# Optimization experiments

Measured on AMD Instinct MI355X. Metric: run time of the kernel, lower is better.

## Reference

```python
import jax, jax.numpy as jnp
import numpy as np

TEMP = 0.5
EPS = 1e-12  # torch F.normalize eps


def setup_inputs() -> dict:
    key = jax.random.key(0)
    k1, k2, k3 = jax.random.split(key, 3)
    B, D = 2048, 128
    z = jax.random.normal(k1, (B, D), dtype=jnp.float32)
    z_aug = jax.random.normal(k2, (B, D), dtype=jnp.float32)
    labels = jax.random.randint(k3, (B,), 0, 2, dtype=jnp.int64)
    return {"z": z, "z_aug": z_aug, "labels": labels}


def _l2_normalize(x):
    n = jnp.linalg.norm(x, axis=1, keepdims=True)
    return x / jnp.maximum(n, EPS)


def _pucon_loss(z, z_aug, labels):
    B = z.shape[0]
    z = _l2_normalize(z)
    z_aug = _l2_normalize(z_aug)

    s00 = (z @ z.T) / TEMP          # [B, B]
    s01 = (z @ z_aug.T) / TEMP
    s10 = (z_aug @ z.T) / TEMP
    s11 = (z_aug @ z_aug.T) / TEMP

    eye = jnp.eye(B, dtype=bool)

    # ---- SelfSupConLoss (reduction='none'): CE over rows with own-diagonal
    # removed from the 00/11 blocks; removal == masking with -inf for CE.
    neg_inf = jnp.array(-jnp.inf, dtype=s00.dtype)
    logits = jnp.concatenate([
        jnp.concatenate([s01, jnp.where(eye, neg_inf, s00)], axis=1),
        jnp.concatenate([s10, jnp.where(eye, neg_inf, s11)], axis=1),
    ], axis=0)                       # [2B, 2B]
    pos = jnp.concatenate([jnp.diagonal(s01), jnp.diagonal(s10)])  # [2B]
    lse = jax.scipy.special.logsumexp(logits, axis=1)
    unsup = lse - pos                # [2B] per-sample NT-Xent loss

    # ---- SupConLoss (reduction='none')
    M = jnp.concatenate([
        jnp.concatenate([s00, s01], axis=1),
        jnp.concatenate([s10, s11], axis=1),
    ], axis=0)                       # [2B, 2B]
    mx = jax.lax.stop_gradient(jnp.max(M, axis=1, keepdims=True))
    Ms = M - mx
    mask = ~jnp.eye(2 * B, dtype=bool)
    e = jnp.where(mask, jnp.exp(Ms), 0.0)
    denom = jnp.sum(e, axis=1, keepdims=True)
    # -log(exp(Ms)/denom) on off-diagonal entries, 0 on diagonal
    nll = jnp.where(mask, jnp.log(denom) - Ms, 0.0)
    eq = labels[:, None] == labels[None, :]
    eq2 = jnp.tile(eq, (2, 2))       # [2B, 2B] bool
    sup = jnp.sum(nll * eq2, axis=1) / (jnp.sum(eq2, axis=1) - 1)  # [2B]

    # ---- PU combination: positives use sup loss, unlabeled use unsup loss
    lab2 = jnp.tile(labels, 2)       # [2B]
    pos_m = (lab2 == 1)
    neg_m = (lab2 == 0)
    n_p = jnp.sum(pos_m)
    n_u = jnp.sum(neg_m)
    total = jnp.maximum(n_p + n_u, 1)
    loss = (jnp.sum(jnp.where(pos_m, sup, 0.0)) +
            jnp.sum(jnp.where(neg_m, unsup, 0.0))) / total
    return jnp.where(n_p == 0, jnp.mean(unsup), loss)


def reference(z, z_aug, labels):
    return _pucon_loss(z, z_aug, labels)
```

## Files before the change

kernel.cpp:

```cpp
#include <hip/hip_runtime.h>
#include <hip/hip_bf16.h>

#define Bsz 2048
#define Dim 128
#define Nrows 4096

typedef float f32x4 __attribute__((ext_vector_type(4)));
typedef __bf16 bf16x8 __attribute__((ext_vector_type(8)));


__global__ __launch_bounds__(256) void k_norm(const float* __restrict__ z,
                                              const float* __restrict__ za,
                                              const long long* __restrict__ labels,
                                              __bf16* __restrict__ U,
                                              float* __restrict__ w1p,
                                              float* __restrict__ wallp,
                                              int* __restrict__ c1out) {
    const int wid = threadIdx.x >> 6, lane = threadIdx.x & 63;
    __shared__ float s1[4][128];
    __shared__ float s0[4][128];
    float a1x = 0.f, a1y = 0.f, a0x = 0.f, a0y = 0.f;
    #pragma unroll
    for (int pass = 0; pass < 4; pass++) {
        const int r = blockIdx.x * 16 + pass * 4 + wid;
        const float* src = (r < Bsz) ? (z + (size_t)r * Dim) : (za + (size_t)(r - Bsz) * Dim);
        float2 x = reinterpret_cast<const float2*>(src)[lane];
        float ss = x.x * x.x + x.y * x.y;
        #pragma unroll
        for (int m = 1; m < 64; m <<= 1) ss += __shfl_xor(ss, m);
        const float sc = 1.0f / fmaxf(sqrtf(ss), 1e-12f);
        const float u0 = x.x * sc, u1 = x.y * sc;
        __bf16* dst = U + (size_t)r * Dim + 2 * lane;
        dst[0] = (__bf16)u0;
        dst[1] = (__bf16)u1;
        const float lf = (labels[r & (Bsz - 1)] == 1) ? 1.f : 0.f;
        a0x += u0; a0y += u1;
        a1x = fmaf(lf, u0, a1x); a1y = fmaf(lf, u1, a1y);
    }
    s1[wid][2 * lane] = a1x; s1[wid][2 * lane + 1] = a1y;
    s0[wid][2 * lane] = a0x; s0[wid][2 * lane + 1] = a0y;
    __syncthreads();
    const int t = threadIdx.x;
    if (t < 128) {
        w1p[blockIdx.x * 128 + t]   = s1[0][t] + s1[1][t] + s1[2][t] + s1[3][t];
        wallp[blockIdx.x * 128 + t] = s0[0][t] + s0[1][t] + s0[2][t] + s0[3][t];
    }
    if (blockIdx.x == 0) {
        __shared__ int ci[256];
        int c = 0;
        #pragma unroll
        for (int k = 0; k < 8; k++) c += (int)labels[t * 8 + k];
        ci[t] = c;
        __syncthreads();
        for (int s = 128; s > 0; s >>= 1) {
            if (t < s) ci[t] += ci[t + s];
            __syncthreads();
        }
        if (t == 0) c1out[0] = ci[0];
    }
}

__global__ __launch_bounds__(256, 2) void k_gram(const __bf16* __restrict__ U,
                                                 const float* __restrict__ w1p,
                                                 const float* __restrict__ wallp,
                                                 float* __restrict__ part,
                                                 float* __restrict__ w1,
                                                 float* __restrict__ wall) {
    if (blockIdx.x == 0) {
        const int t = threadIdx.x;
        const int d = t & 127;
        const float* src = (t < 128) ? w1p : wallp;
        float acc = 0.f;
        #pragma unroll 8
        for (int k = 0; k < 256; k++) acc += src[k * 128 + d];
        if (t < 128) w1[d] = acc; else wall[d] = acc;
        return;
    }

    __shared__ __bf16 Aj0[128 * 128];
    __shared__ __bf16 Aj1[128 * 128];

    const int ib = (blockIdx.x - 1) >> 4;
    const int jc = (blockIdx.x - 1) & 15;
    const int ibase = ib * 128;
    const int jbase0 = jc * 256, jbase1 = jc * 256 + 128;
    const int w = threadIdx.x >> 6, lane = threadIdx.x & 63;
    const int wi = w & 1, wj = w >> 1;
    const int l15 = lane & 15, l4 = lane >> 4;
    const int p = lane & 15, rsub = lane >> 4;

    bf16x8 b[4][4];
    #pragma unroll
    for (int bt = 0; bt < 4; bt++)
        #pragma unroll
        for (int ks = 0; ks < 4; ks++)
            b[bt][ks] = *reinterpret_cast<const bf16x8*>(
                U + (size_t)(ibase + wi * 64 + bt * 16 + l15) * Dim + (ks * 4 + l4) * 8);

    {
        bf16x8 st[8];
        #pragma unroll
        for (int it = 0; it < 8; it++) {
            const int rl = w * 32 + it * 4 + rsub;
            st[it] = *reinterpret_cast<const bf16x8*>(U + (size_t)(jbase0 + rl) * Dim + p * 8);
        }
        #pragma unroll
        for (int it = 0; it < 8; it++) {
            const int rl = w * 32 + it * 4 + rsub;
            *reinterpret_cast<bf16x8*>(Aj0 + (rl * 16 + (p ^ (rl & 7))) * 8) = st[it];
        }
    }
    __syncthreads();

    bf16x8 st1[8];
    #pragma unroll
    for (int it = 0; it < 8; it++) {
        const int rl = w * 32 + it * 4 + rsub;
        st1[it] = *reinterpret_cast<const bf16x8*>(U + (size_t)(jbase1 + rl) * Dim + p * 8);
    }

    const float KE1 = 2.8853900817779268f;
    const float KE0 = -2.8853900817779268f;

    auto compute = [&](const __bf16* Aj, int jbase, int strip) {
        float dsum[4] = {0.f, 0.f, 0.f, 0.f};
        #pragma unroll
        for (int at = 0; at < 4; at++) {
            bf16x8 a[4];
            #pragma unroll
            for (int ks = 0; ks < 4; ks++)
                a[ks] = *reinterpret_cast<const bf16x8*>(
                    Aj + ((wj * 64 + at * 16 + l15) * 16 + ((ks * 4 + l4) ^ (l15 & 7))) * 8);
            const int jt = jbase + wj * 64 + at * 16;
            #pragma unroll
            for (int bt = 0; bt < 4; bt++) {
                f32x4 acc = {0.f, 0.f, 0.f, 0.f};
                #pragma unroll
                for (int ks = 0; ks < 4; ks++)
                    acc = __builtin_amdgcn_mfma_f32_16x16x32_bf16(a[ks], b[bt][ks], acc, 0, 0, 0);
                const bool dg = (jt == ibase + wi * 64 + bt * 16);
                #pragma unroll
                for (int q = 0; q < 4; q++) {
                    float e = exp2f(fmaf(acc[q], KE1, KE0));
                    if (dg && (l15 == l4 * 4 + q)) e = 0.f;
                    dsum[bt] += e;
                }
            }
        }
        #pragma unroll
        for (int bt = 0; bt < 4; bt++) {
            float v0 = dsum[bt];
            v0 += __shfl_xor(v0, 16);
            v0 += __shfl_xor(v0, 32);
            if (l4 == 0)
                part[(ibase + wi * 64 + bt * 16 + l15) * 64 + strip] = v0;
        }
    };

    compute(Aj0, jbase0, jc * 4 + wj);

    #pragma unroll
    for (int it = 0; it < 8; it++) {
        const int rl = w * 32 + it * 4 + rsub;
        *reinterpret_cast<bf16x8*>(Aj1 + (rl * 16 + (p ^ (rl & 7))) * 8) = st1[it];
    }
    __syncthreads();

    compute(Aj1, jbase1, jc * 4 + 2 + wj);
}

__global__ __launch_bounds__(256) void k_row(const __bf16* __restrict__ U,
                                             const long long* __restrict__ labels,
                                             const int* __restrict__ c1p,
                                             const float* __restrict__ part,
                                             const float* __restrict__ w1,
                                             const float* __restrict__ wall,
                                             float* __restrict__ rowC,
                                             float* __restrict__ rowU) {
    const int wid = threadIdx.x >> 6, lane = threadIdx.x & 63;
    const int c1 = *c1p;
    const float w1a = w1[2 * lane], w1b = w1[2 * lane + 1];
    const float wa  = wall[2 * lane], wb = wall[2 * lane + 1];
    float cs = 0.f, us = 0.f;
    #pragma unroll
    for (int rr = 0; rr < 4; rr++) {
        const int i = blockIdx.x * 16 + wid * 4 + rr;
        const int partner = (i < Bsz) ? i + Bsz : i - Bsz;
        float dn = part[i * 64 + lane];
        const float u0 = (float)U[(size_t)i * Dim + 2 * lane];
        const float u1 = (float)U[(size_t)i * Dim + 2 * lane + 1];
        const float p0 = (float)U[(size_t)partner * Dim + 2 * lane];
        const float p1 = (float)U[(size_t)partner * Dim + 2 * lane + 1];
        float d1 = u0 * w1a + u1 * w1b;
        float da = u0 * wa + u1 * wb;
        float ds = u0 * u0 + u1 * u1;
        float dp = u0 * p0 + u1 * p1;
        #pragma unroll
        for (int m = 1; m < 64; m <<= 1) {
            dn += __shfl_xor(dn, m);
            d1 += __shfl_xor(d1, m);
            da += __shfl_xor(da, m);
            ds += __shfl_xor(ds, m);
            dp += __shfl_xor(dp, m);
        }
        if (lane == 0) {
            const long long lb = labels[i & (Bsz - 1)];
            const float lnD = logf(dn) + 2.0f;
            const float uns = lnD - 2.0f * dp;
            const float cnt = 2.f * (float)((lb == 1) ? c1 : (Bsz - c1));
            const float sii = 2.f * ds;
            const float sumeq = ((lb == 1) ? 2.f * d1 : 2.f * (da - d1)) - sii;
            const float sup = lnD - sumeq / (cnt - 1.f);
            cs += (lb == 1) ? sup : uns;
            us += uns;
        }
    }
    __shared__ float wcs[4], wus[4];
    if (lane == 0) { wcs[wid] = cs; wus[wid] = us; }
    __syncthreads();
    if (threadIdx.x == 0) {
        rowC[blockIdx.x] = wcs[0] + wcs[1] + wcs[2] + wcs[3];
        rowU[blockIdx.x] = wus[0] + wus[1] + wus[2] + wus[3];
    }
}

__global__ __launch_bounds__(256) void k_comb(const float* __restrict__ rowC,
                                              const float* __restrict__ rowU,
                                              const int* __restrict__ c1p,
                                              float* __restrict__ out) {
    __shared__ float sc[256], su[256];
    const int t = threadIdx.x;
    sc[t] = rowC[t];
    su[t] = rowU[t];
    __syncthreads();
    for (int s = 128; s > 0; s >>= 1) {
        if (t < s) { sc[t] += sc[t + s]; su[t] += su[t + s]; }
        __syncthreads();
    }
    if (t == 0) out[0] = ((*c1p > 0) ? sc[0] : su[0]) / (float)Nrows;
}

extern "C" void kernel_launch(void* const* d_in, const int* in_sizes, int n_in,
                              void* d_out, int out_size, void* d_ws, size_t ws_size,
                              hipStream_t stream) {
    const float* z  = (const float*)d_in[0];
    const float* za = (const float*)d_in[1];
    const long long* labels = (const long long*)d_in[2];

    char* ws = (char*)d_ws;
    __bf16* U     = (__bf16*)(ws);
    float*  part  = (float*)(ws + (1u << 20));
    float*  w1p   = (float*)(ws + (2u << 20));
    float*  wallp = (float*)(ws + (2u << 20) + (128u << 10));
    float*  w1    = (float*)(ws + (2u << 20) + (256u << 10));
    float*  wall  = (float*)(ws + (2u << 20) + (256u << 10) + 512);
    int*    c1    = (int*)  (ws + (2u << 20) + (256u << 10) + 1024);
    float*  rowC  = (float*)(ws + (2u << 20) + (257u << 10));
    float*  rowU  = (float*)(ws + (2u << 20) + (258u << 10));
    float*  out   = (float*)d_out;

    hipLaunchKernelGGL(k_norm, dim3(256), dim3(256), 0, stream, z, za, labels, U, w1p, wallp, c1);
    hipLaunchKernelGGL(k_gram, dim3(513), dim3(256), 0, stream, U, w1p, wallp, part, w1, wall);
    hipLaunchKernelGGL(k_row,  dim3(256), dim3(256), 0, stream, U, labels, c1, part, w1, wall, rowC, rowU);
    hipLaunchKernelGGL(k_comb, dim3(1),   dim3(256), 0, stream, rowC, rowU, c1, out);
}
```

Before: 31.49 us.

## Enlarge Gram tiles to 256x256 with 512-thread blocks and shared i-tile

The Gram/exp kernel now has each block cover a 256x256 tile with 8 waves instead of a 128x256 strip with 4 waves. Both the i and j row tiles are staged in LDS, and diagonal blocks load the tile only once. The number of per-row partial strips drops from 64 to 32. The row kernel still reads the partials with 64 lanes, so each row's sum counts every strip twice; the log offset changes from 2 to 2 − ln 2 to cancel that doubling. The goal is more operand reuse and fewer global loads, at the cost of half as many blocks, more LDS per block and possibly lower occupancy.

```diff
diff --git a/kernel.cpp b/kernel.cpp
--- a/kernel.cpp
+++ b/kernel.cpp
@@ -60,7 +60,7 @@
     }
 }
 
-__global__ __launch_bounds__(256, 2) void k_gram(const __bf16* __restrict__ U,
+__global__ __launch_bounds__(512, 2) void k_gram(const __bf16* __restrict__ U,
                                                  const float* __restrict__ w1p,
                                                  const float* __restrict__ wallp,
                                                  float* __restrict__ part,
@@ -68,105 +68,107 @@
                                                  float* __restrict__ wall) {
     if (blockIdx.x == 0) {
         const int t = threadIdx.x;
-        const int d = t & 127;
-        const float* src = (t < 128) ? w1p : wallp;
-        float acc = 0.f;
-        #pragma unroll 8
-        for (int k = 0; k < 256; k++) acc += src[k * 128 + d];
-        if (t < 128) w1[d] = acc; else wall[d] = acc;
+        if (t < 256) {
+            const int d = t & 127;
+            const float* src = (t < 128) ? w1p : wallp;
+            float acc = 0.f;
+            #pragma unroll 8
+            for (int k = 0; k < 256; k++) acc += src[k * 128 + d];
+            if (t < 128) w1[d] = acc; else wall[d] = acc;
+        }
         return;
     }
 
-    __shared__ __bf16 Aj0[128 * 128];
-    __shared__ __bf16 Aj1[128 * 128];
-
-    const int ib = (blockIdx.x - 1) >> 4;
-    const int jc = (blockIdx.x - 1) & 15;
-    const int ibase = ib * 128;
-    const int jbase0 = jc * 256, jbase1 = jc * 256 + 128;
+    __shared__ __bf16 Ai[256 * 128];
+    __shared__ __bf16 Aj[256 * 128];
+
+    const int ibk = (blockIdx.x - 1) >> 4, jbk = (blockIdx.x - 1) & 15;
+    const bool diag = (ibk == jbk);
+    const int ibase = ibk * 256, jbase = jbk * 256;
     const int w = threadIdx.x >> 6, lane = threadIdx.x & 63;
-    const int wi = w & 1, wj = w >> 1;
+    const int wiq = w & 3, wjh = w >> 2;
     const int l15 = lane & 15, l4 = lane >> 4;
-    const int p = lane & 15, rsub = lane >> 4;
-
-    bf16x8 b[4][4];
-    #pragma unroll
-    for (int bt = 0; bt < 4; bt++)
-        #pragma unroll
-        for (int ks = 0; ks < 4; ks++)
-            b[bt][ks] = *reinterpret_cast<const bf16x8*>(
-                U + (size_t)(ibase + wi * 64 + bt * 16 + l15) * Dim + (ks * 4 + l4) * 8);
 
     {
-        bf16x8 st[8];
+        const int p = lane & 15, rsub = lane >> 4;
+        bf16x8 sti[8], stj[8];
         #pragma unroll
         for (int it = 0; it < 8; it++) {
             const int rl = w * 32 + it * 4 + rsub;
-            st[it] = *reinterpret_cast<const bf16x8*>(U + (size_t)(jbase0 + rl) * Dim + p * 8);
+            sti[it] = *reinterpret_cast<const bf16x8*>(U + (size_t)(ibase + rl) * Dim + p * 8);
+        }
+        if (!diag) {
+            #pragma unroll
+            for (int it = 0; it < 8; it++) {
+                const int rl = w * 32 + it * 4 + rsub;
+                stj[it] = *reinterpret_cast<const bf16x8*>(U + (size_t)(jbase + rl) * Dim + p * 8);
+            }
         }
         #pragma unroll
         for (int it = 0; it < 8; it++) {
             const int rl = w * 32 + it * 4 + rsub;
-            *reinterpret_cast<bf16x8*>(Aj0 + (rl * 16 + (p ^ (rl & 7))) * 8) = st[it];
-        }
-    }
-    __syncthreads();
-
-    bf16x8 st1[8];
-    #pragma unroll
-    for (int it = 0; it < 8; it++) {
-        const int rl = w * 32 + it * 4 + rsub;
-        st1[it] = *reinterpret_cast<const bf16x8*>(U + (size_t)(jbase1 + rl) * Dim + p * 8);
-    }
-
+            *reinterpret_cast<bf16x8*>(Ai + (rl * 16 + (p ^ (rl & 7))) * 8) = sti[it];
+        }
+        if (!diag) {
+            #pragma unroll
+            for (int it = 0; it < 8; it++) {
+                const int rl = w * 32 + it * 4 + rsub;
+                *reinterpret_cast<bf16x8*>(Aj + (rl * 16 + (p ^ (rl & 7))) * 8) = stj[it];
+            }
+        }
+    }
+    __syncthreads();
+    const __bf16* AjP = diag ? Ai : Aj;
+
+    bf16x8 b[4][4];
+    #pragma unroll
+    for (int bt = 0; bt < 4; bt++)
+        #pragma unroll
+        for (int ks = 0; ks < 4; ks++) {
+            const int row = wiq * 64 + bt * 16 + l15;
+            b[bt][ks] = *reinterpret_cast<const bf16x8*>(
+                Ai + (row * 16 + ((ks * 4 + l4) ^ (row & 7))) * 8);
+        }
+
+    float dsum[4] = {0.f, 0.f, 0.f, 0.f};
     const float KE1 = 2.8853900817779268f;
     const float KE0 = -2.8853900817779268f;
 
-    auto compute = [&](const __bf16* Aj, int jbase, int strip) {
-        float dsum[4] = {0.f, 0.f, 0.f, 0.f};
-        #pragma unroll
-        for (int at = 0; at < 4; at++) {
-            bf16x8 a[4];
+    #pragma unroll
+    for (int at = 0; at < 8; at++) {
+        const int arow = wjh * 128 + at * 16 + l15;
+        bf16x8 a[4];
+        #pragma unroll
+        for (int ks = 0; ks < 4; ks++)
+            a[ks] = *reinterpret_cast<const bf16x8*>(
+                AjP + (arow * 16 + ((ks * 4 + l4) ^ (arow & 7))) * 8);
+        const int jt = jbase + wjh * 128 + at * 16;
+
+        #pragma unroll
+        for (int bt = 0; bt < 4; bt++) {
+            f32x4 acc = {0.f, 0.f, 0.f, 0.f};
             #pragma unroll
             for (int ks = 0; ks < 4; ks++)
-                a[ks] = *reinterpret_cast<const bf16x8*>(
-                    Aj + ((wj * 64 + at * 16 + l15) * 16 + ((ks * 4 + l4) ^ (l15 & 7))) * 8);
-            const int jt = jbase + wj * 64 + at * 16;
-            #pragma unroll
-            for (int bt = 0; bt < 4; bt++) {
-                f32x4 acc = {0.f, 0.f, 0.f, 0.f};
-                #pragma unroll
-                for (int ks = 0; ks < 4; ks++)
-                    acc = __builtin_amdgcn_mfma_f32_16x16x32_bf16(a[ks], b[bt][ks], acc, 0, 0, 0);
-                const bool dg = (jt == ibase + wi * 64 + bt * 16);
-                #pragma unroll
-                for (int q = 0; q < 4; q++) {
-                    float e = exp2f(fmaf(acc[q], KE1, KE0));
-                    if (dg && (l15 == l4 * 4 + q)) e = 0.f;
-                    dsum[bt] += e;
-                }
+                acc = __builtin_amdgcn_mfma_f32_16x16x32_bf16(a[ks], b[bt][ks], acc, 0, 0, 0);
+            const bool dg = (jt == ibase + wiq * 64 + bt * 16);
+            #pragma unroll
+            for (int q = 0; q < 4; q++) {
+                float e = exp2f(fmaf(acc[q], KE1, KE0));
+                if (dg && (l15 == l4 * 4 + q)) e = 0.f;
+                dsum[bt] += e;
             }
         }
-        #pragma unroll
-        for (int bt = 0; bt < 4; bt++) {
-            float v0 = dsum[bt];
-            v0 += __shfl_xor(v0, 16);
-            v0 += __shfl_xor(v0, 32);
-            if (l4 == 0)
-                part[(ibase + wi * 64 + bt * 16 + l15) * 64 + strip] = v0;
-        }
-    };
-
-    compute(Aj0, jbase0, jc * 4 + wj);
-
-    #pragma unroll
-    for (int it = 0; it < 8; it++) {
-        const int rl = w * 32 + it * 4 + rsub;
-        *reinterpret_cast<bf16x8*>(Aj1 + (rl * 16 + (p ^ (rl & 7))) * 8) = st1[it];
-    }
-    __syncthreads();
-
-    compute(Aj1, jbase1, jc * 4 + 2 + wj);
+    }
+
+    const int strip = jbk * 2 + wjh;
+    #pragma unroll
+    for (int bt = 0; bt < 4; bt++) {
+        float v0 = dsum[bt];
+        v0 += __shfl_xor(v0, 16);
+        v0 += __shfl_xor(v0, 32);
+        if (l4 == 0)
+            part[(ibase + wiq * 64 + bt * 16 + l15) * 32 + strip] = v0;
+    }
 }
 
 __global__ __launch_bounds__(256) void k_row(const __bf16* __restrict__ U,
@@ -178,6 +180,7 @@
                                              float* __restrict__ rowC,
                                              float* __restrict__ rowU) {
     const int wid = threadIdx.x >> 6, lane = threadIdx.x & 63;
+    const int ls = lane & 31;
     const int c1 = *c1p;
     const float w1a = w1[2 * lane], w1b = w1[2 * lane + 1];
     const float wa  = wall[2 * lane], wb = wall[2 * lane + 1];
@@ -186,7 +189,7 @@
     for (int rr = 0; rr < 4; rr++) {
         const int i = blockIdx.x * 16 + wid * 4 + rr;
         const int partner = (i < Bsz) ? i + Bsz : i - Bsz;
-        float dn = part[i * 64 + lane];
+        float dn = part[i * 32 + ls];
         const float u0 = (float)U[(size_t)i * Dim + 2 * lane];
         const float u1 = (float)U[(size_t)i * Dim + 2 * lane + 1];
         const float p0 = (float)U[(size_t)partner * Dim + 2 * lane];
@@ -205,7 +208,7 @@
         }
         if (lane == 0) {
             const long long lb = labels[i & (Bsz - 1)];
-            const float lnD = logf(dn) + 2.0f;
+            const float lnD = logf(dn) + 1.30685282f;
             const float uns = lnD - 2.0f * dp;
             const float cnt = 2.f * (float)((lb == 1) ? c1 : (Bsz - c1));
             const float sii = 2.f * ds;
@@ -260,7 +263,7 @@
     float*  out   = (float*)d_out;
 
     hipLaunchKernelGGL(k_norm, dim3(256), dim3(256), 0, stream, z, za, labels, U, w1p, wallp, c1);
-    hipLaunchKernelGGL(k_gram, dim3(513), dim3(256), 0, stream, U, w1p, wallp, part, w1, wall);
+    hipLaunchKernelGGL(k_gram, dim3(257), dim3(512), 0, stream, U, w1p, wallp, part, w1, wall);
     hipLaunchKernelGGL(k_row,  dim3(256), dim3(256), 0, stream, U, labels, c1, part, w1, wall, rowC, rowU);
     hipLaunchKernelGGL(k_comb, dim3(1),   dim3(256), 0, stream, rowC, rowU, c1, out);
 }
```

New measurement: 32.33 us. 2.7% more time.
